# Kernel optimization log

Measured on AMD Instinct MI355X. Metric: run time of the kernel, lower is better.

The kernel has to match this reference:

```python
import jax, jax.numpy as jnp
import numpy as np
import math

B, S, D_IN, D_Q = 4, 2048, 512, 512

def setup_inputs() -> dict:
    key = jax.random.key(0)
    ks = jax.random.split(key, 7)
    s_in = 1.0 / math.sqrt(D_IN)
    x = jax.random.normal(ks[0], (B, S, D_IN), dtype=jnp.float32)
    # nn.Linear-style params: W [out,in], b [out]; uniform(-1/sqrt(in), 1/sqrt(in))
    Wq = jax.random.uniform(ks[1], (D_Q, D_IN), jnp.float32, -s_in, s_in)
    bq = jax.random.uniform(ks[2], (D_Q,), jnp.float32, -s_in, s_in)
    Wk = jax.random.uniform(ks[3], (D_Q, D_IN), jnp.float32, -s_in, s_in)
    bk = jax.random.uniform(ks[4], (D_Q,), jnp.float32, -s_in, s_in)
    Wv = jax.random.uniform(ks[5], (D_Q, D_IN), jnp.float32, -s_in, s_in)
    bv = jax.random.uniform(ks[6], (D_Q,), jnp.float32, -s_in, s_in)
    return {"x": x, "Wq": Wq, "bq": bq, "Wk": Wk, "bk": bk, "Wv": Wv, "bv": bv}

def reference(x, Wq, bq, Wk, bk, Wv, bv):
    # Q/K/V projections: [B,S,D_IN] @ W^T + b -> [B,S,D_Q]
    Q = jnp.einsum('bsi,qi->bsq', x, Wq) + bq
    K = jnp.einsum('bsi,qi->bsq', x, Wk) + bk
    V = jnp.einsum('bsi,qi->bsq', x, Wv) + bv
    scale = 1.0 / math.sqrt(D_Q)
    scores = jnp.einsum('bsq,btq->bst', Q, K) * scale  # [B,S,S]
    attention = jax.nn.softmax(scores, axis=-1)        # 'atten_prob'
    weighted = jnp.einsum('bst,btq->bsq', attention, V)  # 'atten_score'
    return (attention, weighted)
```

## Files before the change

kernel.cpp:

```cpp
#include <hip/hip_runtime.h>
#include <hip/hip_bf16.h>

typedef unsigned short u16;
typedef short bf16x8 __attribute__((ext_vector_type(8)));
typedef float f32x4 __attribute__((ext_vector_type(4)));

#define S_LEN 2048
#define DQ 512
#define NBATCH 4

__device__ __forceinline__ u16 f2bf(float f) {
    __hip_bfloat16 h = __float2bfloat16(f);
    return *reinterpret_cast<u16*>(&h);
}
__device__ __forceinline__ float bf2f(u16 u) {
    unsigned v = ((unsigned)u) << 16;
    union { unsigned u; float f; } c; c.u = v; return c.f;
}

__device__ __forceinline__ void async16(const u16* g, u16* l) {
    __builtin_amdgcn_global_load_lds(
        (__attribute__((address_space(1))) void*)g,
        (__attribute__((address_space(3))) void*)l, 16, 0, 0);
}

__device__ __forceinline__ int xcd_swz(int bid, int chunk) {
    return (bid & 7) * chunk + (bid >> 3);
}

template<int SWAP>
__device__ __forceinline__ f32x4 mm(bf16x8 af, bf16x8 bf, f32x4 c) {
    if constexpr (SWAP)
        return __builtin_amdgcn_mfma_f32_16x16x32_bf16(bf, af, c, 0, 0, 0);
    else
        return __builtin_amdgcn_mfma_f32_16x16x32_bf16(af, bf, c, 0, 0, 0);
}

__global__ __launch_bounds__(256) void k_cvt_all(const float* __restrict__ x,
                                                 const float* __restrict__ wq,
                                                 const float* __restrict__ wk,
                                                 const float* __restrict__ wv,
                                                 u16* __restrict__ xb, u16* __restrict__ wb,
                                                 float* __restrict__ sums) {
    int bid = blockIdx.x;
    if (bid >= 4864) {
        int i = (bid - 4864) * 256 + threadIdx.x;
        *(f32x4*)(sums + (size_t)i * 4) = (f32x4)0.0f;
        return;
    }
    const float* src;
    u16* dst;
    int i;
    if (bid < 4096)      { src = x;  dst = xb;          i = bid * 256 + threadIdx.x; }
    else if (bid < 4352) { src = wq; dst = wb;          i = (bid - 4096) * 256 + threadIdx.x; }
    else if (bid < 4608) { src = wk; dst = wb + 262144; i = (bid - 4352) * 256 + threadIdx.x; }
    else                 { src = wv; dst = wb + 524288; i = (bid - 4608) * 256 + threadIdx.x; }
    f32x4 v = *(const f32x4*)(src + (size_t)i * 4);
    ushort4 o;
    o.x = f2bf(v.x); o.y = f2bf(v.y); o.z = f2bf(v.z); o.w = f2bf(v.w);
    *(ushort4*)(dst + (size_t)i * 4) = o;
}

__device__ __forceinline__ void stage_unit(const u16* __restrict__ G, u16* buf,
                                           int kcol, int h, int tid) {
#pragma unroll
    for (int q = 0; q < 2; ++q) {
        int c   = q * 512 + tid;
        int r   = c >> 3;
        int p   = c & 7;
        int lch = p ^ (r & 7);
        async16(G + (size_t)(h * 128 + r) * DQ + kcol + lch * 8,
                buf + h * 8192 + c * 8);
    }
}

template<int SWAP>
__device__ __forceinline__ void gemm256(const u16* __restrict__ A, const u16* __restrict__ B,
                                        u16* ldsA, u16* ldsB, f32x4 acc[8][4], int tid) {
    const int lane = tid & 63;
    const int w    = tid >> 6;
    const int wr   = w >> 2;
    const int wc   = w & 3;
    const int l16  = lane & 15;
    const int quad = lane >> 4;
    const int p0   = quad ^ (l16 & 7);
    const int a0   = (wr * 128 + l16) * 64 + p0 * 8;
    const int a1   = (wr * 128 + l16) * 64 + (p0 ^ 4) * 8;
    const int b0   = (wc * 64 + l16) * 64 + p0 * 8;
    const int b1   = (wc * 64 + l16) * 64 + (p0 ^ 4) * 8;

    stage_unit(A, ldsA, 0, 0, tid);
    stage_unit(A, ldsA, 0, 1, tid);
    stage_unit(B, ldsB, 0, 0, tid);
    stage_unit(B, ldsB, 0, 1, tid);
    __syncthreads();

    for (int kt = 0; kt < 8; ++kt) {
        const u16* rdA = ldsA + (kt & 1) * 16384;
        const u16* rdB = ldsB + (kt & 1) * 16384;
        u16* wrA = ldsA + ((kt + 1) & 1) * 16384;
        u16* wrB = ldsB + ((kt + 1) & 1) * 16384;
        const int  kc = (kt + 1) * 64;
        const bool pf = kt < 7;
        bf16x8 a[4][2], bbf[2][2];

        if (pf) { stage_unit(A, wrA, kc, 0, tid); stage_unit(A, wrA, kc, 1, tid); }
#pragma unroll
        for (int i = 0; i < 4; ++i) {
            a[i][0] = *(const bf16x8*)(rdA + a0 + i * 1024);
            a[i][1] = *(const bf16x8*)(rdA + a1 + i * 1024);
        }
#pragma unroll
        for (int j = 0; j < 2; ++j) {
            bbf[j][0] = *(const bf16x8*)(rdB + b0 + j * 1024);
            bbf[j][1] = *(const bf16x8*)(rdB + b1 + j * 1024);
        }
        __builtin_amdgcn_s_setprio(1);
#pragma unroll
        for (int i = 0; i < 4; ++i)
#pragma unroll
            for (int j = 0; j < 2; ++j) {
                acc[i][j] = mm<SWAP>(a[i][0], bbf[j][0], acc[i][j]);
                acc[i][j] = mm<SWAP>(a[i][1], bbf[j][1], acc[i][j]);
            }
        __builtin_amdgcn_s_setprio(0);

        if (pf) { stage_unit(B, wrB, kc, 0, tid); stage_unit(B, wrB, kc, 1, tid); }
#pragma unroll
        for (int j = 0; j < 2; ++j) {
            bbf[j][0] = *(const bf16x8*)(rdB + b0 + (2 + j) * 1024);
            bbf[j][1] = *(const bf16x8*)(rdB + b1 + (2 + j) * 1024);
        }
        __builtin_amdgcn_s_setprio(1);
#pragma unroll
        for (int i = 0; i < 4; ++i)
#pragma unroll
            for (int j = 0; j < 2; ++j) {
                acc[i][2 + j] = mm<SWAP>(a[i][0], bbf[j][0], acc[i][2 + j]);
                acc[i][2 + j] = mm<SWAP>(a[i][1], bbf[j][1], acc[i][2 + j]);
            }
        __builtin_amdgcn_s_setprio(0);

#pragma unroll
        for (int i = 0; i < 4; ++i) {
            a[i][0] = *(const bf16x8*)(rdA + a0 + (4 + i) * 1024);
            a[i][1] = *(const bf16x8*)(rdA + a1 + (4 + i) * 1024);
        }
        __builtin_amdgcn_s_setprio(1);
#pragma unroll
        for (int i = 0; i < 4; ++i)
#pragma unroll
            for (int j = 0; j < 2; ++j) {
                acc[4 + i][2 + j] = mm<SWAP>(a[i][0], bbf[j][0], acc[4 + i][2 + j]);
                acc[4 + i][2 + j] = mm<SWAP>(a[i][1], bbf[j][1], acc[4 + i][2 + j]);
            }
        __builtin_amdgcn_s_setprio(0);

#pragma unroll
        for (int j = 0; j < 2; ++j) {
            bbf[j][0] = *(const bf16x8*)(rdB + b0 + j * 1024);
            bbf[j][1] = *(const bf16x8*)(rdB + b1 + j * 1024);
        }
        __builtin_amdgcn_s_setprio(1);
#pragma unroll
        for (int i = 0; i < 4; ++i)
#pragma unroll
            for (int j = 0; j < 2; ++j) {
                acc[4 + i][j] = mm<SWAP>(a[i][0], bbf[j][0], acc[4 + i][j]);
                acc[4 + i][j] = mm<SWAP>(a[i][1], bbf[j][1], acc[4 + i][j]);
            }
        __builtin_amdgcn_s_setprio(0);

        __syncthreads();
    }
}

__global__ __launch_bounds__(512, 2) void k_proj(const u16* __restrict__ xb, const u16* __restrict__ Wb,
                                                 const float* __restrict__ bq, const float* __restrict__ bk,
                                                 const float* __restrict__ bv, u16* __restrict__ out,
                                                 u16* __restrict__ VT) {
    __shared__ __align__(16) u16 lds[65536];
    const int l  = xcd_swz(blockIdx.x, 24);
    const int bx = l & 1;
    const int by = (l >> 1) & 31;
    const int z  = l >> 6;
    const int m0 = by * 256, n0 = bx * 256;
    const u16* A = xb + (size_t)m0 * DQ;
    const u16* B = Wb + (size_t)z * DQ * DQ + (size_t)n0 * DQ;
    const float* bias = (z == 0) ? bq : (z == 1) ? bk : bv;

    f32x4 acc[8][4];
#pragma unroll
    for (int i = 0; i < 8; ++i)
#pragma unroll
        for (int j = 0; j < 4; ++j) acc[i][j] = (f32x4)0.0f;

    const int tid = threadIdx.x;
    gemm256<0>(A, B, lds, lds + 32768, acc, tid);

    const int lane = tid & 63, w = tid >> 6;
    const int wr = w >> 2, wc = w & 3;
    const int l16 = lane & 15, quad = lane >> 4;

    if (z < 2) {
        u16* outz = out + (size_t)z * 8192 * DQ;
#pragma unroll
        for (int j = 0; j < 4; ++j) {
            int gn = n0 + wc * 64 + j * 16 + l16;
            float bv_ = bias[gn];
#pragma unroll
            for (int i = 0; i < 8; ++i)
#pragma unroll
                for (int r = 0; r < 4; ++r) {
                    int gm = m0 + wr * 128 + i * 16 + quad * 4 + r;
                    outz[(size_t)gm * DQ + gn] = f2bf(acc[i][j][r] + bv_);
                }
        }
    } else {
        const int bb_ = m0 >> 11;
        u16* VTb_ = VT + (size_t)bb_ * DQ * S_LEN;
#pragma unroll
        for (int j = 0; j < 4; ++j) {
            int gn = n0 + wc * 64 + j * 16 + l16;
            float bv_ = bias[gn];
#pragma unroll
            for (int i = 0; i < 8; ++i) {
                int t0 = (m0 & 2047) + wr * 128 + i * 16 + quad * 4;
                ushort4 o;
                o.x = f2bf(acc[i][j][0] + bv_);
                o.y = f2bf(acc[i][j][1] + bv_);
                o.z = f2bf(acc[i][j][2] + bv_);
                o.w = f2bf(acc[i][j][3] + bv_);
                *(ushort4*)(VTb_ + (size_t)gn * S_LEN + t0) = o;
            }
        }
    }
}

__global__ __launch_bounds__(512, 2) void k_scores(const u16* __restrict__ Qb, const u16* __restrict__ Kb,
                                                   u16* __restrict__ Pb, float* __restrict__ sums) {
    __shared__ __align__(16) u16 lds[65536];
    const int l  = xcd_swz(blockIdx.x, 32);
    const int bx = l & 7;
    const int by = (l >> 3) & 7;
    const int b  = l >> 6;
    const int m0 = by * 256, n0 = bx * 256;
    const u16* A = Qb + ((size_t)b * S_LEN + m0) * DQ;
    const u16* B = Kb + ((size_t)b * S_LEN + n0) * DQ;

    f32x4 acc[8][4];
#pragma unroll
    for (int i = 0; i < 8; ++i)
#pragma unroll
        for (int j = 0; j < 4; ++j) acc[i][j] = (f32x4)0.0f;

    const int tid = threadIdx.x;
    gemm256<1>(A, B, lds, lds + 32768, acc, tid);

    const float scale = 0.044194173824159216f;
    const int lane = tid & 63, w = tid >> 6;
    const int wr = w >> 2, wc = w & 3;
    const int l16 = lane & 15, quad = lane >> 4;
    u16* prow = Pb + (size_t)(b * S_LEN + m0) * S_LEN;
    float* sums_row = sums + b * S_LEN + m0 + wr * 128;

#pragma unroll
    for (int i = 0; i < 8; ++i) {
        float ps = 0.0f;
        const size_t rowoff = (size_t)(wr * 128 + i * 16 + l16) * S_LEN;
#pragma unroll
        for (int j = 0; j < 4; ++j) {
            ushort4 o;
            o.x = f2bf(__expf(acc[i][j][0] * scale));
            o.y = f2bf(__expf(acc[i][j][1] * scale));
            o.z = f2bf(__expf(acc[i][j][2] * scale));
            o.w = f2bf(__expf(acc[i][j][3] * scale));
            *(ushort4*)(prow + rowoff + n0 + wc * 64 + j * 16 + quad * 4) = o;
            ps += (bf2f(o.x) + bf2f(o.y)) + (bf2f(o.z) + bf2f(o.w));
        }
        ps += __shfl_xor(ps, 16);
        ps += __shfl_xor(ps, 32);
        if (quad == 0) atomicAdd(&sums_row[i * 16 + l16], ps);
    }
}

__device__ __forceinline__ void stage_pv(const u16* __restrict__ G, u16* buf,
                                         int kcol, int h, int tid) {
    int c   = tid;
    int r   = c >> 3;
    int p   = c & 7;
    int lch = p ^ (r & 7);
    async16(G + (size_t)(h * 64 + r) * S_LEN + kcol + lch * 8,
            buf + h * 4096 + c * 8);
}

__global__ __launch_bounds__(512, 2) void k_pv(const u16* __restrict__ Pb, const u16* __restrict__ VT,
                                               const float* __restrict__ sums,
                                               float* __restrict__ probs,
                                               float* __restrict__ wout) {
    __shared__ __align__(16) u16 lds[49408];
    u16* ldsA = lds;
    u16* ldsB = lds + 24576;
    float* ldsInv = (float*)(lds + 49152);
    const int l  = xcd_swz(blockIdx.x, 32);
    const int bx = l & 3;
    const int by = (l >> 2) & 15;
    const int b  = l >> 6;
    const int m0 = by * 128, n0 = bx * 128;
    const u16* A = Pb + (size_t)(b * S_LEN + m0) * S_LEN;
    const u16* B = VT + (size_t)b * DQ * S_LEN + (size_t)n0 * S_LEN;
    const u16* Psl = Pb + (size_t)(b * S_LEN + m0) * S_LEN + bx * 512;
    float* Pro = probs + ((size_t)b * S_LEN + m0) * S_LEN + bx * 512;

    const int tid  = threadIdx.x;
    const int lane = tid & 63;
    const int w    = tid >> 6;
    const int wr   = w >> 2;
    const int wc   = w & 3;
    const int l16  = lane & 15;
    const int quad = lane >> 4;
    const int p0   = quad ^ (l16 & 7);
    const int a0   = (wr * 64 + l16) * 64 + p0 * 8;
    const int a1   = (wr * 64 + l16) * 64 + (p0 ^ 4) * 8;
    const int b0   = (wc * 32 + l16) * 64 + p0 * 8;
    const int b1   = (wc * 32 + l16) * 64 + (p0 ^ 4) * 8;

    f32x4 acc[4][2];
#pragma unroll
    for (int i = 0; i < 4; ++i)
#pragma unroll
        for (int j = 0; j < 2; ++j) acc[i][j] = (f32x4)0.0f;

    float sv = 1.0f;
    if (tid < 128) sv = sums[b * S_LEN + m0 + tid];
    stage_pv(A, ldsA, 0, 0, tid);          stage_pv(A, ldsA, 0, 1, tid);
    stage_pv(B, ldsB, 0, 0, tid);          stage_pv(B, ldsB, 0, 1, tid);
    stage_pv(A, ldsA + 8192, 64, 0, tid);  stage_pv(A, ldsA + 8192, 64, 1, tid);
    stage_pv(B, ldsB + 8192, 64, 0, tid);  stage_pv(B, ldsB + 8192, 64, 1, tid);
    if (tid < 128) ldsInv[tid] = 1.0f / sv;
    asm volatile("s_waitcnt vmcnt(4) lgkmcnt(0)" ::: "memory");
    __builtin_amdgcn_s_barrier();
    __builtin_amdgcn_sched_barrier(0);

    int rb = 0;
    for (int kt = 0; kt < 32; ++kt) {
        const u16* rdA = ldsA + rb * 8192;
        const u16* rdB = ldsB + rb * 8192;

        const bool do_probs = (kt & 1) == 0;
        bf16x8 pvv;
        float pinv = 0.0f;
        float* pdst = nullptr;
        if (do_probs) {
            int idx = (kt >> 1) * 512 + tid;
            int r  = idx >> 6;
            int cc = (idx & 63) << 3;
            pvv  = *(const bf16x8*)(Psl + (size_t)r * S_LEN + cc);
            pinv = ldsInv[r];
            pdst = Pro + (size_t)r * S_LEN + cc;
        }

        if (kt < 30) {
            int wbi = rb >= 1 ? rb - 1 : 2;
            u16* wA = ldsA + wbi * 8192;
            u16* wB = ldsB + wbi * 8192;
            const int kc = (kt + 2) * 64;
            stage_pv(A, wA, kc, 0, tid);
            stage_pv(A, wA, kc, 1, tid);
            stage_pv(B, wB, kc, 0, tid);
            stage_pv(B, wB, kc, 1, tid);
        }

        bf16x8 a[4][2], bbf[2];
#pragma unroll
        for (int i = 0; i < 4; ++i) {
            a[i][0] = *(const bf16x8*)(rdA + a0 + i * 1024);
            a[i][1] = *(const bf16x8*)(rdA + a1 + i * 1024);
        }
        bbf[0] = *(const bf16x8*)(rdB + b0);
        bbf[1] = *(const bf16x8*)(rdB + b1);
        __builtin_amdgcn_s_setprio(1);
#pragma unroll
        for (int i = 0; i < 4; ++i) {
            acc[i][0] = __builtin_amdgcn_mfma_f32_16x16x32_bf16(a[i][0], bbf[0], acc[i][0], 0, 0, 0);
            acc[i][0] = __builtin_amdgcn_mfma_f32_16x16x32_bf16(a[i][1], bbf[1], acc[i][0], 0, 0, 0);
        }
        __builtin_amdgcn_s_setprio(0);

        bbf[0] = *(const bf16x8*)(rdB + b0 + 1024);
        bbf[1] = *(const bf16x8*)(rdB + b1 + 1024);
        __builtin_amdgcn_s_setprio(1);
#pragma unroll
        for (int i = 0; i < 4; ++i) {
            acc[i][1] = __builtin_amdgcn_mfma_f32_16x16x32_bf16(a[i][0], bbf[0], acc[i][1], 0, 0, 0);
            acc[i][1] = __builtin_amdgcn_mfma_f32_16x16x32_bf16(a[i][1], bbf[1], acc[i][1], 0, 0, 0);
        }
        __builtin_amdgcn_s_setprio(0);

        if (do_probs) {
            f32x4 o0, o1;
            o0.x = bf2f((u16)pvv[0]) * pinv;
            o0.y = bf2f((u16)pvv[1]) * pinv;
            o0.z = bf2f((u16)pvv[2]) * pinv;
            o0.w = bf2f((u16)pvv[3]) * pinv;
            o1.x = bf2f((u16)pvv[4]) * pinv;
            o1.y = bf2f((u16)pvv[5]) * pinv;
            o1.z = bf2f((u16)pvv[6]) * pinv;
            o1.w = bf2f((u16)pvv[7]) * pinv;
            *(f32x4*)(pdst) = o0;
            *(f32x4*)(pdst + 4) = o1;
        }

        if (kt < 31) {
            if (kt < 30) asm volatile("s_waitcnt vmcnt(6)" ::: "memory");
            else         asm volatile("s_waitcnt vmcnt(2)" ::: "memory");
            __builtin_amdgcn_s_barrier();
            __builtin_amdgcn_sched_barrier(0);
        }
        rb = (rb == 2) ? 0 : rb + 1;
    }

    float* outb = wout + (size_t)b * S_LEN * DQ;
#pragma unroll
    for (int i = 0; i < 4; ++i) {
#pragma unroll
        for (int r = 0; r < 4; ++r) {
            int lm = wr * 64 + i * 16 + quad * 4 + r;
            float inv = ldsInv[lm];
#pragma unroll
            for (int j = 0; j < 2; ++j) {
                int gn = n0 + wc * 32 + j * 16 + l16;
                outb[(size_t)(m0 + lm) * DQ + gn] = acc[i][j][r] * inv;
            }
        }
    }
}

extern "C" void kernel_launch(void* const* d_in, const int* in_sizes, int n_in,
                              void* d_out, int out_size, void* d_ws, size_t ws_size,
                              hipStream_t stream) {
    const float* x  = (const float*)d_in[0];
    const float* Wq = (const float*)d_in[1];
    const float* bq = (const float*)d_in[2];
    const float* Wk = (const float*)d_in[3];
    const float* bk = (const float*)d_in[4];
    const float* Wv = (const float*)d_in[5];
    const float* bv = (const float*)d_in[6];

    char* ws = (char*)d_ws;
    u16* xb  = (u16*)(ws);
    u16* Wb  = (u16*)(ws + 8388608);
    u16* Qb  = (u16*)(ws + 9961472);
    u16* Kb  = (u16*)(ws + 18350080);
    u16* VTb = (u16*)(ws + 35127296);
    u16* Pb  = (u16*)(ws + 43515904);
    float* sums = (float*)(ws + 77070336);
    float* probs = (float*)d_out;
    float* wout  = (float*)d_out + 16777216;

    k_cvt_all<<<4872, 256, 0, stream>>>(x, Wq, Wk, Wv, xb, Wb, sums);
    k_proj<<<192, 512, 0, stream>>>(xb, Wb, bq, bk, bv, Qb, VTb);
    k_scores<<<256, 512, 0, stream>>>(Qb, Kb, Pb, sums);
    k_pv<<<256, 512, 0, stream>>>(Pb, VTb, sums, probs, wout);
}
```

Baseline: 174.2 us.

## Retile scores GEMM to 128x128 blocks with triple-buffered LDS pipeline

The QK^T scores kernel moves from 256x256 tiles (256 blocks) to 128x128 tiles (1024 blocks). Its main loop is now a dedicated triple-buffered async global-to-LDS pipeline with a 64-wide K step, swizzled LDS addressing and setprio around the MFMA bursts. The aim is better occupancy and load balance across CUs, since 256 blocks barely fill the GPU. The cost is lower data reuse per tile, which doubles the global reads of Q and K.

Measured after the change: 183.1 us. 1.05x slower.

```diff
diff --git a/kernel.cpp b/kernel.cpp
--- a/kernel.cpp
+++ b/kernel.cpp
@@ -237,45 +237,123 @@
     }
 }
 
+__device__ __forceinline__ void stage_sc(const u16* __restrict__ G, u16* buf,
+                                         int kcol, int h, int tid) {
+    int c   = tid;
+    int r   = c >> 3;
+    int p   = c & 7;
+    int lch = p ^ (r & 7);
+    async16(G + (size_t)(h * 64 + r) * DQ + kcol + lch * 8,
+            buf + h * 4096 + c * 8);
+}
+
 __global__ __launch_bounds__(512, 2) void k_scores(const u16* __restrict__ Qb, const u16* __restrict__ Kb,
                                                    u16* __restrict__ Pb, float* __restrict__ sums) {
-    __shared__ __align__(16) u16 lds[65536];
-    const int l  = xcd_swz(blockIdx.x, 32);
-    const int bx = l & 7;
-    const int by = (l >> 3) & 7;
-    const int b  = l >> 6;
-    const int m0 = by * 256, n0 = bx * 256;
+    __shared__ __align__(16) u16 lds[49152];
+    u16* ldsA = lds;
+    u16* ldsB = lds + 24576;
+    const int l  = xcd_swz(blockIdx.x, 128);
+    const int bx = l & 15;
+    const int by = (l >> 4) & 15;
+    const int b  = l >> 8;
+    const int m0 = by * 128, n0 = bx * 128;
     const u16* A = Qb + ((size_t)b * S_LEN + m0) * DQ;
     const u16* B = Kb + ((size_t)b * S_LEN + n0) * DQ;
 
-    f32x4 acc[8][4];
-#pragma unroll
-    for (int i = 0; i < 8; ++i)
-#pragma unroll
-        for (int j = 0; j < 4; ++j) acc[i][j] = (f32x4)0.0f;
-
-    const int tid = threadIdx.x;
-    gemm256<1>(A, B, lds, lds + 32768, acc, tid);
+    const int tid  = threadIdx.x;
+    const int lane = tid & 63;
+    const int w    = tid >> 6;
+    const int wr   = w >> 2;
+    const int wc   = w & 3;
+    const int l16  = lane & 15;
+    const int quad = lane >> 4;
+    const int p0   = quad ^ (l16 & 7);
+    const int a0   = (wr * 64 + l16) * 64 + p0 * 8;
+    const int a1   = (wr * 64 + l16) * 64 + (p0 ^ 4) * 8;
+    const int b0   = (wc * 32 + l16) * 64 + p0 * 8;
+    const int b1   = (wc * 32 + l16) * 64 + (p0 ^ 4) * 8;
+
+    f32x4 acc[4][2];
+#pragma unroll
+    for (int i = 0; i < 4; ++i)
+#pragma unroll
+        for (int j = 0; j < 2; ++j) acc[i][j] = (f32x4)0.0f;
+
+    stage_sc(A, ldsA, 0, 0, tid);          stage_sc(A, ldsA, 0, 1, tid);
+    stage_sc(B, ldsB, 0, 0, tid);          stage_sc(B, ldsB, 0, 1, tid);
+    stage_sc(A, ldsA + 8192, 64, 0, tid);  stage_sc(A, ldsA + 8192, 64, 1, tid);
+    stage_sc(B, ldsB + 8192, 64, 0, tid);  stage_sc(B, ldsB + 8192, 64, 1, tid);
+    asm volatile("s_waitcnt vmcnt(4)" ::: "memory");
+    __builtin_amdgcn_s_barrier();
+    __builtin_amdgcn_sched_barrier(0);
+
+    int rb = 0;
+    for (int kt = 0; kt < 8; ++kt) {
+        const u16* rdA = ldsA + rb * 8192;
+        const u16* rdB = ldsB + rb * 8192;
+
+        if (kt < 6) {
+            int wbi = rb >= 1 ? rb - 1 : 2;
+            u16* wA = ldsA + wbi * 8192;
+            u16* wB = ldsB + wbi * 8192;
+            const int kc = (kt + 2) * 64;
+            stage_sc(A, wA, kc, 0, tid);
+            stage_sc(A, wA, kc, 1, tid);
+            stage_sc(B, wB, kc, 0, tid);
+            stage_sc(B, wB, kc, 1, tid);
+        }
+
+        bf16x8 a[4][2], bbf[2];
+#pragma unroll
+        for (int i = 0; i < 4; ++i) {
+            a[i][0] = *(const bf16x8*)(rdA + a0 + i * 1024);
+            a[i][1] = *(const bf16x8*)(rdA + a1 + i * 1024);
+        }
+        bbf[0] = *(const bf16x8*)(rdB + b0);
+        bbf[1] = *(const bf16x8*)(rdB + b1);
+        __builtin_amdgcn_s_setprio(1);
+#pragma unroll
+        for (int i = 0; i < 4; ++i) {
+            acc[i][0] = mm<1>(a[i][0], bbf[0], acc[i][0]);
+            acc[i][0] = mm<1>(a[i][1], bbf[1], acc[i][0]);
+        }
+        __builtin_amdgcn_s_setprio(0);
+
+        bbf[0] = *(const bf16x8*)(rdB + b0 + 1024);
+        bbf[1] = *(const bf16x8*)(rdB + b1 + 1024);
+        __builtin_amdgcn_s_setprio(1);
+#pragma unroll
+        for (int i = 0; i < 4; ++i) {
+            acc[i][1] = mm<1>(a[i][0], bbf[0], acc[i][1]);
+            acc[i][1] = mm<1>(a[i][1], bbf[1], acc[i][1]);
+        }
+        __builtin_amdgcn_s_setprio(0);
+
+        if (kt < 7) {
+            if (kt < 6) asm volatile("s_waitcnt vmcnt(4)" ::: "memory");
+            else        asm volatile("s_waitcnt vmcnt(0)" ::: "memory");
+            __builtin_amdgcn_s_barrier();
+            __builtin_amdgcn_sched_barrier(0);
+        }
+        rb = (rb == 2) ? 0 : rb + 1;
+    }
 
     const float scale = 0.044194173824159216f;
-    const int lane = tid & 63, w = tid >> 6;
-    const int wr = w >> 2, wc = w & 3;
-    const int l16 = lane & 15, quad = lane >> 4;
     u16* prow = Pb + (size_t)(b * S_LEN + m0) * S_LEN;
-    float* sums_row = sums + b * S_LEN + m0 + wr * 128;
-
-#pragma unroll
-    for (int i = 0; i < 8; ++i) {
+    float* sums_row = sums + b * S_LEN + m0 + wr * 64;
+
+#pragma unroll
+    for (int i = 0; i < 4; ++i) {
         float ps = 0.0f;
-        const size_t rowoff = (size_t)(wr * 128 + i * 16 + l16) * S_LEN;
-#pragma unroll
-        for (int j = 0; j < 4; ++j) {
+        const size_t rowoff = (size_t)(wr * 64 + i * 16 + l16) * S_LEN;
+#pragma unroll
+        for (int j = 0; j < 2; ++j) {
             ushort4 o;
             o.x = f2bf(__expf(acc[i][j][0] * scale));
             o.y = f2bf(__expf(acc[i][j][1] * scale));
             o.z = f2bf(__expf(acc[i][j][2] * scale));
             o.w = f2bf(__expf(acc[i][j][3] * scale));
-            *(ushort4*)(prow + rowoff + n0 + wc * 64 + j * 16 + quad * 4) = o;
+            *(ushort4*)(prow + rowoff + n0 + wc * 32 + j * 16 + quad * 4) = o;
             ps += (bf2f(o.x) + bf2f(o.y)) + (bf2f(o.z) + bf2f(o.w));
         }
         ps += __shfl_xor(ps, 16);
@@ -460,6 +538,6 @@
 
     k_cvt_all<<<4872, 256, 0, stream>>>(x, Wq, Wk, Wv, xb, Wb, sums);
     k_proj<<<192, 512, 0, stream>>>(xb, Wb, bq, bk, bv, Qb, VTb);
-    k_scores<<<256, 512, 0, stream>>>(Qb, Kb, Pb, sums);
+    k_scores<<<1024, 512, 0, stream>>>(Qb, Kb, Pb, sums);
     k_pv<<<256, 512, 0, stream>>>(Pb, VTb, sums, probs, wout);
 }
```
